# Performance work log

Hardware: AMD Instinct MI355X
Metric: run time of the kernel (lower is better)

Reference implementation:

```python
import jax, jax.numpy as jnp
import numpy as np

N = 50000      # nodes
E = 800000     # edges
IN = 128       # in_channels
H = 128        # hidden_channels
L = 3          # num_layers
CONF_H = 64    # confidence_hidden_dim
TAU0 = 1.0


def _linear_params(key, fan_in, fan_out, bias=True):
    k1, k2 = jax.random.split(key)
    lim = 1.0 / np.sqrt(fan_in)
    w = jax.random.uniform(k1, (fan_in, fan_out), jnp.float32, -lim, lim)
    if bias:
        b = jax.random.uniform(k2, (fan_out,), jnp.float32, -lim, lim)
        return w, b
    return w


def setup_inputs() -> dict:
    key = jax.random.key(0)
    ks = jax.random.split(key, 20)
    x = jax.random.normal(ks[0], (N, IN), jnp.float32)
    edge_index = jax.random.randint(ks[1], (2, E), 0, N, jnp.int32)
    gnoise_soft = jax.random.gumbel(ks[2], (L, N, 2), jnp.float32)
    gnoise_hard = jax.random.gumbel(ks[3], (L, N, 2), jnp.float32)
    conv_w0, conv_b0 = _linear_params(ks[4], IN, H)
    conv_w1, conv_b1 = _linear_params(ks[5], H, H)
    conv_w2, conv_b2 = _linear_params(ks[6], H, H)
    soft_w1, soft_b1 = _linear_params(ks[7], H, CONF_H)
    soft_w2, soft_b2 = _linear_params(ks[8], CONF_H, 2)
    hard_w1, hard_b1 = _linear_params(ks[9], H + 1, CONF_H)
    hard_w2, hard_b2 = _linear_params(ks[10], CONF_H, 2)
    temp_w = _linear_params(ks[11], H, 1, bias=False)
    return dict(x=x, edge_index=edge_index, gnoise_soft=gnoise_soft, gnoise_hard=gnoise_hard,
                conv_w0=conv_w0, conv_b0=conv_b0, conv_w1=conv_w1, conv_b1=conv_b1,
                conv_w2=conv_w2, conv_b2=conv_b2,
                soft_w1=soft_w1, soft_b1=soft_b1, soft_w2=soft_w2, soft_b2=soft_b2,
                hard_w1=hard_w1, hard_b1=hard_b1, hard_w2=hard_w2, hard_b2=hard_b2,
                temp_w=temp_w)


def _forward(x, edge_index, gnoise_soft, gnoise_hard,
             conv_w0, conv_b0, conv_w1, conv_b1, conv_w2, conv_b2,
             soft_w1, soft_b1, soft_w2, soft_b2,
             hard_w1, hard_b1, hard_w2, hard_b2, temp_w):
    src, dst = edge_index[0], edge_index[1]
    loop = jnp.arange(N, dtype=src.dtype)
    # GCN symmetric normalization with self-loops (PyG gcn_norm)
    src_sl = jnp.concatenate([src, loop])
    dst_sl = jnp.concatenate([dst, loop])
    deg = jax.ops.segment_sum(jnp.ones(E + N, x.dtype), dst_sl, num_segments=N)
    dinv = jnp.where(deg > 0, jax.lax.rsqrt(deg), 0.0)
    norm = dinv[src_sl] * dinv[dst_sl]  # [E+N]
    # readiness graph: self-loops removed
    nonself = (src != dst).astype(x.dtype)
    deg_ns = jnp.clip(jax.ops.segment_sum(nonself, src, num_segments=N), 1.0)

    conv_params = [(conv_w0, conv_b0), (conv_w1, conv_b1), (conv_w2, conv_b2)]
    z = jnp.zeros((N, H), x.dtype)
    soft_exited = jnp.zeros(N, bool)
    hard_exited = jnp.zeros(N, bool)
    exit_layers = jnp.full((N,), L, jnp.int32)
    active = []
    h = x
    for li in range(L):
        W, b = conv_params[li]
        hw = h @ W  # [N,H]
        h = jax.ops.segment_sum(norm[:, None] * hw[src_sl], dst_sl, num_segments=N) + b
        if li < L - 1:
            h = jax.nn.gelu(h, approximate=False)  # torch F.gelu default (dropout p=0)
        active.append(jnp.sum(~hard_exited).astype(jnp.int32))
        # temperature head: 1 / (softplus(Wx) + tau0)
        temp = 1.0 / (jax.nn.softplus(h @ temp_w) + TAU0)  # [N,1]
        temp = jnp.where(jnp.isinf(temp), 0.0, temp)
        # soft exit head + gumbel softmax (hard=False)
        soft_logits = jax.nn.relu(h @ soft_w1 + soft_b1) @ soft_w2 + soft_b2  # [N,2]
        sg = jax.nn.softmax((soft_logits + gnoise_soft[li]) / temp, axis=-1)
        soft_dec = sg[:, 1] > sg[:, 0]
        soft_exited = soft_exited | (soft_dec & ~soft_exited)
        # neighbor readiness: mean of soft_exited over non-self neighbors (detached)
        ready_sum = jax.ops.segment_sum(soft_exited[dst].astype(x.dtype) * nonself, src, num_segments=N)
        readiness = jax.lax.stop_gradient((ready_sum / deg_ns)[:, None])
        hin = jnp.concatenate([h, readiness], axis=-1)  # [N,H+1]
        hard_logits = jax.nn.relu(hin @ hard_w1 + hard_b1) @ hard_w2 + hard_b2
        cont = jnp.concatenate([jnp.full((N, 1), 1e6, x.dtype), jnp.zeros((N, 1), x.dtype)], axis=-1)
        eff = jnp.where(soft_exited[:, None], hard_logits, cont)
        hg = jax.nn.softmax((eff + gnoise_hard[li]) / temp, axis=-1)
        hard_dec = hg[:, 1] > hg[:, 0]
        newly = hard_dec & ~hard_exited
        z = z + h * newly[:, None].astype(x.dtype)
        exit_layers = jnp.where(newly, jnp.int32(li), exit_layers)
        hard_exited = hard_exited | newly
    z = z + h * (~hard_exited)[:, None].astype(x.dtype)
    return z, exit_layers, jnp.stack(active)


def reference(x, edge_index, gnoise_soft, gnoise_hard,
              conv_w0, conv_b0, conv_w1, conv_b1, conv_w2, conv_b2,
              soft_w1, soft_b1, soft_w2, soft_b2,
              hard_w1, hard_b1, hard_w2, hard_b2, temp_w):
    return _forward(x, edge_index, gnoise_soft, gnoise_hard,
                    conv_w0, conv_b0, conv_w1, conv_b1, conv_w2, conv_b2,
                    soft_w1, soft_b1, soft_w2, soft_b2,
                    hard_w1, hard_b1, hard_w2, hard_b2, temp_w)
```

## Files before the change

kernel.cpp:

```cpp
#include <hip/hip_runtime.h>
#include <hip/hip_bf16.h>
#include <math.h>

#define NN 50000
#define EE 800000
#define HH 128
#define CHH 64
#define LL 3
#define ZT (NN * HH)
#define NBK 196
#define EPB 3125

using bf16 = __hip_bfloat16;
typedef unsigned short u16;
typedef unsigned int u32;
typedef __attribute__((ext_vector_type(8))) short s16x8;
typedef __attribute__((ext_vector_type(4))) float f32x4;

__device__ __forceinline__ float ldbf(const u16* p, size_t i) {
    return __uint_as_float(((u32)p[i]) << 16);
}
__device__ __forceinline__ u16 f2b(float v) {
    bf16 b = __float2bfloat16(v);
    return *reinterpret_cast<u16*>(&b);
}
__device__ __forceinline__ void stbf(u16* p, size_t i, float v) { p[i] = f2b(v); }
__device__ __forceinline__ float blo(u32 w) { return __uint_as_float(w << 16); }
__device__ __forceinline__ float bhi(u32 w) { return __uint_as_float(w & 0xFFFF0000u); }

__global__ __launch_bounds__(256) void zero_out_k(float* __restrict__ out, int n) {
    int i = blockIdx.x * 256 + threadIdx.x;
    if (i < n) out[i] = 0.f;
}

__global__ __launch_bounds__(256) void init_k(const float* __restrict__ x, u16* __restrict__ h,
        int* __restrict__ softex, int* __restrict__ hardex, int* __restrict__ exitl,
        int* __restrict__ act) {
    int i = blockIdx.x * 256 + threadIdx.x;
    if (i < ZT) stbf(h, (size_t)i, x[i]);
    if (i < NN) { softex[i] = 0; hardex[i] = 0; exitl[i] = LL; }
    if (i < LL) act[i] = 0;
}

__global__ __launch_bounds__(256) void hist_both_k(const int* __restrict__ ei,
        int* __restrict__ hist1, int* __restrict__ hist2) {
    __shared__ int h1[NBK], h2[NBK];
    int t = threadIdx.x, b = blockIdx.x;
    if (t < NBK) { h1[t] = 0; h2[t] = 0; }
    __syncthreads();
    int base = b * EPB;
    for (int i = t; i < EPB; i += 256) {
        int e = base + i;
        int s = ei[e], d = ei[EE + e];
        if ((u32)s >= NN || (u32)d >= NN) continue;
        atomicAdd(&h1[d >> 8], 1);
        if (s != d) atomicAdd(&h2[s >> 8], 1);
    }
    __syncthreads();
    if (t < NBK) { hist1[b * NBK + t] = h1[t]; hist2[b * NBK + t] = h2[t]; }
}

__global__ __launch_bounds__(256) void boffs_k(const int* __restrict__ hist,
        int* __restrict__ boffs, int* __restrict__ bstart) {
    int t = threadIdx.x;
    __shared__ int scn[256];
    int run = 0;
    if (t < NBK) {
        for (int b = 0; b < 256; ++b) {
            boffs[t * 256 + b] = run;
            run += hist[b * NBK + t];
        }
    }
    int v = (t < NBK) ? run : 0;
    scn[t] = v;
    __syncthreads();
    for (int off = 1; off < 256; off <<= 1) {
        int x = (t >= off) ? scn[t - off] : 0;
        __syncthreads();
        scn[t] += x;
        __syncthreads();
    }
    int excl = scn[t] - v;
    if (t < NBK) {
        bstart[t] = excl;
        if (t == NBK - 1) bstart[NBK] = excl + v;
        for (int b = 0; b < 256; ++b) boffs[t * 256 + b] += excl;
    }
}

__global__ __launch_bounds__(256) void scat_both_k(const int* __restrict__ ei,
        const int* __restrict__ boffs1, u32* __restrict__ ebuf1,
        const int* __restrict__ boffs2, u32* __restrict__ ebuf2) {
    __shared__ int c1[NBK], c2[NBK];
    int t = threadIdx.x, b = blockIdx.x;
    if (t < NBK) { c1[t] = boffs1[t * 256 + b]; c2[t] = boffs2[t * 256 + b]; }
    __syncthreads();
    int base = b * EPB;
    for (int i = t; i < EPB; i += 256) {
        int e = base + i;
        int s = ei[e], d = ei[EE + e];
        if ((u32)s >= NN || (u32)d >= NN) continue;
        int pos = atomicAdd(&c1[d >> 8], 1);
        ebuf1[pos] = (u32)s | ((u32)(d & 255) << 16);
        if (s != d) {
            int pos2 = atomicAdd(&c2[s >> 8], 1);
            ebuf2[pos2] = (u32)d | ((u32)(s & 255) << 16);
        }
    }
}

__device__ __forceinline__ void fine_body(int bk, const u32* __restrict__ ebuf,
        const int* __restrict__ bstart, int* __restrict__ rowptr, u16* __restrict__ csrx,
        float* __restrict__ dinv, int addself) {
    __shared__ int cnt[256];
    __shared__ int scn[256];
    int t = threadIdx.x;
    int eb = bstart[bk], ee = bstart[bk + 1];
    cnt[t] = 0;
    __syncthreads();
    for (int i = eb + t; i < ee; i += 256)
        atomicAdd(&cnt[(ebuf[i] >> 16) & 255], 1);
    __syncthreads();
    int v = cnt[t];
    scn[t] = v;
    __syncthreads();
    for (int off = 1; off < 256; off <<= 1) {
        int x = (t >= off) ? scn[t - off] : 0;
        __syncthreads();
        scn[t] += x;
        __syncthreads();
    }
    int excl = scn[t] - v;
    int n = (bk << 8) + t;
    if (n < NN) {
        rowptr[n] = eb + excl;
        if (dinv) dinv[n] = 1.0f / sqrtf((float)(v + addself));
    }
    if (bk == NBK - 1 && t == 0) rowptr[NN] = ee;
    __syncthreads();
    cnt[t] = excl;
    __syncthreads();
    for (int i = eb + t; i < ee; i += 256) {
        u32 w = ebuf[i];
        int lo = (w >> 16) & 255;
        int pos = atomicAdd(&cnt[lo], 1);
        csrx[eb + pos] = (u16)(w & 0xFFFF);
    }
}

__global__ __launch_bounds__(256) void fine2_k(const u32* __restrict__ ebuf1,
        const int* __restrict__ bstart1, int* __restrict__ irow, u16* __restrict__ csrc,
        float* __restrict__ dinv, const u32* __restrict__ ebuf2,
        const int* __restrict__ bstart2, int* __restrict__ orow, u16* __restrict__ ocol) {
    if (blockIdx.x < NBK) fine_body(blockIdx.x, ebuf1, bstart1, irow, csrc, dinv, 1);
    else                  fine_body(blockIdx.x - NBK, ebuf2, bstart2, orow, ocol, nullptr, 0);
}

__global__ __launch_bounds__(256) void pack_w_k(const float* __restrict__ w0,
        const float* __restrict__ w1, const float* __restrict__ w2,
        const float* __restrict__ sw1, const float* __restrict__ hw1, u16* __restrict__ wt) {
    int i = blockIdx.x * 256 + threadIdx.x;
    if (i >= 4 * HH * HH) return;
    int mat = i >> 14, rr = i & 16383, o = rr >> 7, k = rr & 127;
    float v;
    if (mat == 0) v = w0[k * HH + o];
    else if (mat == 1) v = w1[k * HH + o];
    else if (mat == 2) v = w2[k * HH + o];
    else v = (o < CHH) ? sw1[k * CHH + o] : hw1[k * CHH + (o - CHH)];
    stbf(wt, (size_t)i, v);
}

__global__ __launch_bounds__(256) void mega_k(int li, int geluf,
        const int* __restrict__ irow, const u16* __restrict__ csrc, const float* __restrict__ dinv,
        const u16* __restrict__ hin_g, u16* __restrict__ hout_g,
        const u16* __restrict__ Wc, const u16* __restrict__ Wh, const float* __restrict__ bias,
        const float* __restrict__ sb1, const float* __restrict__ sw2, const float* __restrict__ sb2,
        const float* __restrict__ gs, int* __restrict__ softex, const int* __restrict__ hardex,
        float* __restrict__ outP) {
    __shared__ u32 hin[16 * 64];
    __shared__ u16 hl[16 * HH];
    __shared__ float l0s[2][16], l1s[2][16];
    __shared__ int hx[16];
    int tid = threadIdx.x;
    int wave = tid >> 6, lane = tid & 63;
    int row0 = blockIdx.x * 16;
    if (tid < 16) hx[tid] = hardex[row0 + tid];
    #pragma unroll
    for (int i = 0; i < 4; ++i) {
        int row = wave * 4 + i;
        int node = row0 + row;
        int beg = irow[node], end = irow[node + 1];
        float dvd = dinv[node];
        float a0 = 0.f, a1 = 0.f;
        int e = beg;
        for (; e + 3 < end; e += 4) {
            int s0 = csrc[e], s1 = csrc[e + 1], s2 = csrc[e + 2], s3 = csrc[e + 3];
            float n0 = dinv[s0], n1 = dinv[s1], n2 = dinv[s2], n3 = dinv[s3];
            u32 w0 = *(const u32*)(hin_g + (size_t)s0 * HH + lane * 2);
            u32 w1 = *(const u32*)(hin_g + (size_t)s1 * HH + lane * 2);
            u32 w2 = *(const u32*)(hin_g + (size_t)s2 * HH + lane * 2);
            u32 w3 = *(const u32*)(hin_g + (size_t)s3 * HH + lane * 2);
            a0 = fmaf(n0, blo(w0), a0); a1 = fmaf(n0, bhi(w0), a1);
            a0 = fmaf(n1, blo(w1), a0); a1 = fmaf(n1, bhi(w1), a1);
            a0 = fmaf(n2, blo(w2), a0); a1 = fmaf(n2, bhi(w2), a1);
            a0 = fmaf(n3, blo(w3), a0); a1 = fmaf(n3, bhi(w3), a1);
        }
        for (; e < end; ++e) {
            int s0 = csrc[e];
            float n0 = dinv[s0];
            u32 w0 = *(const u32*)(hin_g + (size_t)s0 * HH + lane * 2);
            a0 = fmaf(n0, blo(w0), a0); a1 = fmaf(n0, bhi(w0), a1);
        }
        a0 *= dvd; a1 *= dvd;
        u32 hw = *(const u32*)(hin_g + (size_t)node * HH + lane * 2);
        float self = dvd * dvd;
        a0 = fmaf(blo(hw), self, a0);
        a1 = fmaf(bhi(hw), self, a1);
        hin[row * 64 + (((lane >> 2) ^ (row & 7)) << 2) + (lane & 3)] =
            (u32)f2b(a0) | ((u32)f2b(a1) << 16);
    }
    __syncthreads();
    int r = lane & 15, g = lane >> 4;
    const u16* hinw = (const u16*)hin;
    s16x8 af[4];
    #pragma unroll
    for (int kk = 0; kk < 4; ++kk) {
        int chunk = (kk * 4 + g) ^ (r & 7);
        af[kk] = *(const s16x8*)(hinw + r * HH + chunk * 8);
    }
    f32x4 acc[2];
    #pragma unroll
    for (int cc = 0; cc < 2; ++cc) {
        int c0 = wave * 32 + cc * 16;
        const u16* brow = Wc + (size_t)(c0 + r) * HH;
        f32x4 a = {0.f, 0.f, 0.f, 0.f};
        #pragma unroll
        for (int kk = 0; kk < 4; ++kk) {
            s16x8 b = *(const s16x8*)(brow + kk * 32 + g * 8);
            a = __builtin_amdgcn_mfma_f32_16x16x32_bf16(af[kk], b, a, 0, 0, 0);
        }
        acc[cc] = a;
    }
    #pragma unroll
    for (int cc = 0; cc < 2; ++cc) {
        int col = wave * 32 + cc * 16 + r;
        float bv = bias[col];
        #pragma unroll
        for (int j = 0; j < 4; ++j) {
            int row = g * 4 + j;
            float v = acc[cc][j] + bv;
            if (geluf) v = 0.5f * v * (1.0f + erff(v * 0.70710678118654752f));
            stbf(hout_g, (size_t)(row0 + row) * HH + col, v);
            int chunk = (col >> 3) ^ (row & 7);
            hl[row * HH + chunk * 8 + (col & 7)] = f2b(v);
        }
    }
    __syncthreads();
    #pragma unroll
    for (int kk = 0; kk < 4; ++kk) {
        int k0 = kk * 32 + g * 8;
        int chunk = (k0 >> 3) ^ (r & 7);
        af[kk] = *(const s16x8*)(hl + r * HH + chunk * 8);
    }
    #pragma unroll
    for (int cc = 0; cc < 2; ++cc) {
        int c0 = wave * 32 + cc * 16;
        const u16* brow = Wh + (size_t)(c0 + r) * HH;
        f32x4 a = {0.f, 0.f, 0.f, 0.f};
        #pragma unroll
        for (int kk = 0; kk < 4; ++kk) {
            s16x8 b = *(const s16x8*)(brow + kk * 32 + g * 8);
            a = __builtin_amdgcn_mfma_f32_16x16x32_bf16(af[kk], b, a, 0, 0, 0);
        }
        acc[cc] = a;
    }
    if (wave < 2) {
        float pl0[4] = {0.f, 0.f, 0.f, 0.f}, pl1[4] = {0.f, 0.f, 0.f, 0.f};
        #pragma unroll
        for (int cc = 0; cc < 2; ++cc) {
            int col = wave * 32 + cc * 16 + r;
            float b1 = sb1[col], w20 = sw2[col * 2], w21 = sw2[col * 2 + 1];
            #pragma unroll
            for (int j = 0; j < 4; ++j) {
                float hv = fmaxf(acc[cc][j] + b1, 0.f);
                pl0[j] = fmaf(hv, w20, pl0[j]);
                pl1[j] = fmaf(hv, w21, pl1[j]);
            }
        }
        #pragma unroll
        for (int off = 1; off < 16; off <<= 1) {
            #pragma unroll
            for (int j = 0; j < 4; ++j) {
                pl0[j] += __shfl_xor(pl0[j], off);
                pl1[j] += __shfl_xor(pl1[j], off);
            }
        }
        if (r == 0) {
            #pragma unroll
            for (int j = 0; j < 4; ++j) {
                l0s[wave][g * 4 + j] = pl0[j];
                l1s[wave][g * 4 + j] = pl1[j];
            }
        }
    } else {
        #pragma unroll
        for (int cc = 0; cc < 2; ++cc) {
            int col = wave * 32 + cc * 16 + r;
            #pragma unroll
            for (int j = 0; j < 4; ++j) {
                int row = g * 4 + j;
                if (!hx[row]) outP[(size_t)(row0 + row) * HH + col] = acc[cc][j];
            }
        }
    }
    __syncthreads();
    if (tid < 16) {
        int n = row0 + tid;
        float l0 = l0s[0][tid] + l0s[1][tid] + sb2[0];
        float l1 = l1s[0][tid] + l1s[1][tid] + sb2[1];
        const float* gg = gs + ((size_t)li * NN + n) * 2;
        if (l1 + gg[1] > l0 + gg[0]) softex[n] = 1;
    }
}

__global__ __launch_bounds__(256) void hard_fin_k(int li,
        const u16* __restrict__ h, const float* __restrict__ hw1, const float* __restrict__ hb1,
        const float* __restrict__ hw2, const float* __restrict__ hb2,
        const float* __restrict__ gh, const int* __restrict__ softex,
        int* __restrict__ hardex, int* __restrict__ exitl,
        const int* __restrict__ orow, const u16* __restrict__ ocol,
        float* __restrict__ out) {
    int t = threadIdx.x;
    int n = blockIdx.x * 4 + (t >> 6);
    int j = t & 63;
    if (!softex[n] || hardex[n]) return;
    int ob = orow[n], oe = orow[n + 1];
    int cnt = 0;
    for (int e = ob + j; e < oe; e += 64) cnt += softex[ocol[e]];
    #pragma unroll
    for (int off = 32; off > 0; off >>= 1) cnt += __shfl_xor(cnt, off);
    int dns = oe - ob; if (dns < 1) dns = 1;
    float r = (float)cnt / (float)dns;
    float pv = out[(size_t)n * HH + CHH + j];
    float hid = fmaxf(pv + r * hw1[HH * CHH + j] + hb1[j], 0.f);
    float l0 = hid * hw2[j * 2], l1 = hid * hw2[j * 2 + 1];
    #pragma unroll
    for (int off = 32; off > 0; off >>= 1) {
        l0 += __shfl_xor(l0, off);
        l1 += __shfl_xor(l1, off);
    }
    const float* g = gh + ((size_t)li * NN + n) * 2;
    if (l1 + hb2[1] + g[1] > l0 + hb2[0] + g[0]) {
        if (j == 0) { hardex[n] = 1; exitl[n] = li; }
        u32 hw = *(const u32*)(h + (size_t)n * HH + j * 2);
        out[(size_t)n * HH + j * 2]     = blo(hw);
        out[(size_t)n * HH + j * 2 + 1] = bhi(hw);
    }
}

__global__ __launch_bounds__(256) void tail_k(const u16* __restrict__ h, const int* __restrict__ exitl,
        float* __restrict__ out, int* __restrict__ act) {
    __shared__ int c[LL];
    int t = threadIdx.x;
    int i = blockIdx.x * 256 + t;
    if (t < LL) c[t] = 0;
    __syncthreads();
    if (i < ZT) {
        int n = i >> 7;
        if (exitl[n] == LL) out[i] = ldbf(h, (size_t)i);
    } else if (i < ZT + NN) {
        int e = exitl[i - ZT];
        out[i] = (float)e;
        if (e < LL) atomicAdd(&c[e], 1);
    }
    __syncthreads();
    if (t < LL && c[t]) atomicAdd(&act[t], c[t]);
}

__global__ __launch_bounds__(64) void finalize_k(const int* __restrict__ act, float* __restrict__ out) {
    if (threadIdx.x == 0) {
        out[ZT + NN]     = (float)NN;
        out[ZT + NN + 1] = (float)(NN - act[0]);
        out[ZT + NN + 2] = (float)(NN - act[0] - act[1]);
    }
}

extern "C" void kernel_launch(void* const* d_in, const int* in_sizes, int n_in,
                              void* d_out, int out_size, void* d_ws, size_t ws_size,
                              hipStream_t stream) {
    float* out = (float*)d_out;
    const int OUT_N = ZT + NN + LL;

    static const int CANON[19] = {6400000,1600000,300000,300000,16384,128,16384,128,16384,128,
                                  8192,64,128,2,8256,64,128,2,128};
    static const int SORTED_ROLE[19] = {5,7,9,4,6,8,1,3,2,15,17,14,16,11,13,10,12,18,0};
    int perm[19];
    bool ok = (n_in == 19);
    if (ok) {
        bool mc = true, mr = true, ms = true;
        for (int i = 0; i < 19; ++i) {
            if (in_sizes[i] != CANON[i]) mc = false;
            if (in_sizes[i] != CANON[18 - i]) mr = false;
            if (in_sizes[i] != CANON[SORTED_ROLE[i]]) ms = false;
        }
        if (mc)      for (int c = 0; c < 19; ++c) perm[c] = c;
        else if (mr) for (int c = 0; c < 19; ++c) perm[c] = 18 - c;
        else if (ms) { for (int p = 0; p < 19; ++p) perm[SORTED_ROLE[p]] = p; }
        else         for (int c = 0; c < 19; ++c) perm[c] = c;
    }
    if (!ok) {
        zero_out_k<<<(OUT_N + 255) / 256, 256, 0, stream>>>(out, OUT_N);
        return;
    }

    const float* x  = (const float*)d_in[perm[0]];
    const int*   ei = (const int*)d_in[perm[1]];
    const float* gs = (const float*)d_in[perm[2]];
    const float* gh = (const float*)d_in[perm[3]];
    const float* cw[3] = { (const float*)d_in[perm[4]], (const float*)d_in[perm[6]], (const float*)d_in[perm[8]] };
    const float* cb[3] = { (const float*)d_in[perm[5]], (const float*)d_in[perm[7]], (const float*)d_in[perm[9]] };
    const float* sw1 = (const float*)d_in[perm[10]];
    const float* sb1 = (const float*)d_in[perm[11]];
    const float* sw2 = (const float*)d_in[perm[12]];
    const float* sb2 = (const float*)d_in[perm[13]];
    const float* hw1 = (const float*)d_in[perm[14]];
    const float* hb1 = (const float*)d_in[perm[15]];
    const float* hw2 = (const float*)d_in[perm[16]];
    const float* hb2 = (const float*)d_in[perm[17]];

    const size_t H_B    = (size_t)ZT * 2;
    const size_t FLAG_B = 200192;
    const size_t ACT_B  = 256;
    const size_t RP_B   = 200704;
    const size_t CE_B   = (size_t)EE * 2;
    const size_t WT_B   = 4 * HH * HH * 2;
    const size_t need = 2 * H_B + 4 * FLAG_B + ACT_B + 2 * RP_B + 2 * CE_B + WT_B;
    if (ws_size < need) {
        zero_out_k<<<(OUT_N + 255) / 256, 256, 0, stream>>>(out, OUT_N);
        return;
    }

    char* p = (char*)d_ws;
    u16* hA   = (u16*)p; p += H_B;
    u16* hB   = (u16*)p; p += H_B;
    int* softex = (int*)p; p += FLAG_B;
    int* hardex = (int*)p; p += FLAG_B;
    int* exitl  = (int*)p; p += FLAG_B;
    float* dinv = (float*)p; p += FLAG_B;
    int* act    = (int*)p; p += ACT_B;
    int* irow   = (int*)p; p += RP_B;
    int* orow   = (int*)p; p += RP_B;
    u16* csrc   = (u16*)p; p += CE_B;
    u16* ocol   = (u16*)p; p += CE_B;
    u16* wt     = (u16*)p; p += WT_B;

    char* q = (char*)hB;
    u32* ebuf1  = (u32*)q;  q += (size_t)EE * 4;
    u32* ebuf2  = (u32*)q;  q += (size_t)EE * 4;
    int* hist1  = (int*)q;  q += 256 * NBK * 4;
    int* hist2  = (int*)q;  q += 256 * NBK * 4;
    int* boffs1 = (int*)q;  q += NBK * 256 * 4;
    int* boffs2 = (int*)q;  q += NBK * 256 * 4;
    int* bstart1 = (int*)q; q += 1024;
    int* bstart2 = (int*)q; q += 1024;

    init_k<<<(ZT + 255) / 256, 256, 0, stream>>>(x, hA, softex, hardex, exitl, act);

    hist_both_k<<<256, 256, 0, stream>>>(ei, hist1, hist2);
    boffs_k<<<1, 256, 0, stream>>>(hist1, boffs1, bstart1);
    boffs_k<<<1, 256, 0, stream>>>(hist2, boffs2, bstart2);
    scat_both_k<<<256, 256, 0, stream>>>(ei, boffs1, ebuf1, boffs2, ebuf2);
    fine2_k<<<2 * NBK, 256, 0, stream>>>(ebuf1, bstart1, irow, csrc, dinv,
                                         ebuf2, bstart2, orow, ocol);
    pack_w_k<<<(4 * HH * HH + 255) / 256, 256, 0, stream>>>(cw[0], cw[1], cw[2], sw1, hw1, wt);

    u16* hbuf[2] = { hA, hB };
    for (int li = 0; li < LL; ++li) {
        int geluf = (li < LL - 1) ? 1 : 0;
        u16* hin  = hbuf[li & 1];
        u16* hout = hbuf[(li & 1) ^ 1];
        mega_k<<<NN / 16, 256, 0, stream>>>(li, geluf, irow, csrc, dinv, hin, hout,
                                            wt + (size_t)li * HH * HH, wt + (size_t)3 * HH * HH,
                                            cb[li], sb1, sw2, sb2, gs, softex, hardex, out);
        hard_fin_k<<<NN / 4, 256, 0, stream>>>(li, hout, hw1, hb1, hw2, hb2, gh, softex,
                                               hardex, exitl, orow, ocol, out);
    }
    tail_k<<<(OUT_N + 255) / 256, 256, 0, stream>>>(hbuf[LL & 1], exitl, out, act);
    finalize_k<<<1, 64, 0, stream>>>(act, out);
}
```

Before: 366.2 us.

## Split fused gather+GEMM into column-quartered gather kernel and separate GEMM kernel

The per-layer fused kernel is split in two. A standalone gather kernel aggregates neighbour features, with each block handling 16 nodes and one 32-column quarter so that adjacent blocks share a column slice, which should improve cache locality of the random row reads. The aggregated rows go to a global buffer, and a second kernel runs the MFMA GEMM and heads from it. This adds an extra global write and read of the aggregated features plus one launch per layer, and lets the feature buffer be updated in place instead of ping-ponging.

```diff
diff --git a/kernel.cpp b/kernel.cpp
--- a/kernel.cpp
+++ b/kernel.cpp
@@ -170,14 +170,54 @@
     stbf(wt, (size_t)i, v);
 }
 
-__global__ __launch_bounds__(256) void mega_k(int li, int geluf,
-        const int* __restrict__ irow, const u16* __restrict__ csrc, const float* __restrict__ dinv,
-        const u16* __restrict__ hin_g, u16* __restrict__ hout_g,
+__global__ __launch_bounds__(256) void gather4_k(const int* __restrict__ irow,
+        const u16* __restrict__ csrc, const float* __restrict__ dinv,
+        const u16* __restrict__ hg, u16* __restrict__ hinb) {
+    int bid = blockIdx.x;
+    int c8 = bid & 7;
+    int q = c8 >> 1;
+    int idx = (bid >> 3) * 2 + (c8 & 1);
+    if (idx >= NN / 16) return;
+    int t = threadIdx.x;
+    int node = idx * 16 + (t >> 4);
+    int l = t & 15;
+    int co = q * 32 + l * 2;
+    int beg = irow[node], end = irow[node + 1];
+    float dvd = dinv[node];
+    float a0 = 0.f, a1 = 0.f;
+    int e = beg;
+    for (; e + 3 < end; e += 4) {
+        int s0 = csrc[e], s1 = csrc[e + 1], s2 = csrc[e + 2], s3 = csrc[e + 3];
+        float n0 = dinv[s0], n1 = dinv[s1], n2 = dinv[s2], n3 = dinv[s3];
+        u32 w0 = *(const u32*)(hg + (size_t)s0 * HH + co);
+        u32 w1 = *(const u32*)(hg + (size_t)s1 * HH + co);
+        u32 w2 = *(const u32*)(hg + (size_t)s2 * HH + co);
+        u32 w3 = *(const u32*)(hg + (size_t)s3 * HH + co);
+        a0 = fmaf(n0, blo(w0), a0); a1 = fmaf(n0, bhi(w0), a1);
+        a0 = fmaf(n1, blo(w1), a0); a1 = fmaf(n1, bhi(w1), a1);
+        a0 = fmaf(n2, blo(w2), a0); a1 = fmaf(n2, bhi(w2), a1);
+        a0 = fmaf(n3, blo(w3), a0); a1 = fmaf(n3, bhi(w3), a1);
+    }
+    for (; e < end; ++e) {
+        int s0 = csrc[e];
+        float n0 = dinv[s0];
+        u32 w0 = *(const u32*)(hg + (size_t)s0 * HH + co);
+        a0 = fmaf(n0, blo(w0), a0); a1 = fmaf(n0, bhi(w0), a1);
+    }
+    a0 *= dvd; a1 *= dvd;
+    u32 hw = *(const u32*)(hg + (size_t)node * HH + co);
+    float self = dvd * dvd;
+    a0 = fmaf(blo(hw), self, a0);
+    a1 = fmaf(bhi(hw), self, a1);
+    ((u32*)hinb)[(size_t)node * 64 + q * 16 + l] = (u32)f2b(a0) | ((u32)f2b(a1) << 16);
+}
+
+__global__ __launch_bounds__(256) void gemmheads_k(int li, int geluf,
+        const u16* __restrict__ hinb, u16* __restrict__ hout_g,
         const u16* __restrict__ Wc, const u16* __restrict__ Wh, const float* __restrict__ bias,
         const float* __restrict__ sb1, const float* __restrict__ sw2, const float* __restrict__ sb2,
         const float* __restrict__ gs, int* __restrict__ softex, const int* __restrict__ hardex,
         float* __restrict__ outP) {
-    __shared__ u32 hin[16 * 64];
     __shared__ u16 hl[16 * HH];
     __shared__ float l0s[2][16], l1s[2][16];
     __shared__ int hx[16];
@@ -185,49 +225,11 @@
     int wave = tid >> 6, lane = tid & 63;
     int row0 = blockIdx.x * 16;
     if (tid < 16) hx[tid] = hardex[row0 + tid];
-    #pragma unroll
-    for (int i = 0; i < 4; ++i) {
-        int row = wave * 4 + i;
-        int node = row0 + row;
-        int beg = irow[node], end = irow[node + 1];
-        float dvd = dinv[node];
-        float a0 = 0.f, a1 = 0.f;
-        int e = beg;
-        for (; e + 3 < end; e += 4) {
-            int s0 = csrc[e], s1 = csrc[e + 1], s2 = csrc[e + 2], s3 = csrc[e + 3];
-            float n0 = dinv[s0], n1 = dinv[s1], n2 = dinv[s2], n3 = dinv[s3];
-            u32 w0 = *(const u32*)(hin_g + (size_t)s0 * HH + lane * 2);
-            u32 w1 = *(const u32*)(hin_g + (size_t)s1 * HH + lane * 2);
-            u32 w2 = *(const u32*)(hin_g + (size_t)s2 * HH + lane * 2);
-            u32 w3 = *(const u32*)(hin_g + (size_t)s3 * HH + lane * 2);
-            a0 = fmaf(n0, blo(w0), a0); a1 = fmaf(n0, bhi(w0), a1);
-            a0 = fmaf(n1, blo(w1), a0); a1 = fmaf(n1, bhi(w1), a1);
-            a0 = fmaf(n2, blo(w2), a0); a1 = fmaf(n2, bhi(w2), a1);
-            a0 = fmaf(n3, blo(w3), a0); a1 = fmaf(n3, bhi(w3), a1);
-        }
-        for (; e < end; ++e) {
-            int s0 = csrc[e];
-            float n0 = dinv[s0];
-            u32 w0 = *(const u32*)(hin_g + (size_t)s0 * HH + lane * 2);
-            a0 = fmaf(n0, blo(w0), a0); a1 = fmaf(n0, bhi(w0), a1);
-        }
-        a0 *= dvd; a1 *= dvd;
-        u32 hw = *(const u32*)(hin_g + (size_t)node * HH + lane * 2);
-        float self = dvd * dvd;
-        a0 = fmaf(blo(hw), self, a0);
-        a1 = fmaf(bhi(hw), self, a1);
-        hin[row * 64 + (((lane >> 2) ^ (row & 7)) << 2) + (lane & 3)] =
-            (u32)f2b(a0) | ((u32)f2b(a1) << 16);
-    }
-    __syncthreads();
     int r = lane & 15, g = lane >> 4;
-    const u16* hinw = (const u16*)hin;
+    const u16* arow = hinb + (size_t)(row0 + r) * HH;
     s16x8 af[4];
     #pragma unroll
-    for (int kk = 0; kk < 4; ++kk) {
-        int chunk = (kk * 4 + g) ^ (r & 7);
-        af[kk] = *(const s16x8*)(hinw + r * HH + chunk * 8);
-    }
+    for (int kk = 0; kk < 4; ++kk) af[kk] = *(const s16x8*)(arow + kk * 32 + g * 8);
     f32x4 acc[2];
     #pragma unroll
     for (int cc = 0; cc < 2; ++cc) {
@@ -441,8 +443,8 @@
     }
 
     char* p = (char*)d_ws;
-    u16* hA   = (u16*)p; p += H_B;
-    u16* hB   = (u16*)p; p += H_B;
+    u16* h    = (u16*)p; p += H_B;
+    u16* hinb = (u16*)p; p += H_B;
     int* softex = (int*)p; p += FLAG_B;
     int* hardex = (int*)p; p += FLAG_B;
     int* exitl  = (int*)p; p += FLAG_B;
@@ -454,7 +456,7 @@
     u16* ocol   = (u16*)p; p += CE_B;
     u16* wt     = (u16*)p; p += WT_B;
 
-    char* q = (char*)hB;
+    char* q = (char*)hinb;
     u32* ebuf1  = (u32*)q;  q += (size_t)EE * 4;
     u32* ebuf2  = (u32*)q;  q += (size_t)EE * 4;
     int* hist1  = (int*)q;  q += 256 * NBK * 4;
@@ -464,7 +466,7 @@
     int* bstart1 = (int*)q; q += 1024;
     int* bstart2 = (int*)q; q += 1024;
 
-    init_k<<<(ZT + 255) / 256, 256, 0, stream>>>(x, hA, softex, hardex, exitl, act);
+    init_k<<<(ZT + 255) / 256, 256, 0, stream>>>(x, h, softex, hardex, exitl, act);
 
     hist_both_k<<<256, 256, 0, stream>>>(ei, hist1, hist2);
     boffs_k<<<1, 256, 0, stream>>>(hist1, boffs1, bstart1);
@@ -474,17 +476,16 @@
                                          ebuf2, bstart2, orow, ocol);
     pack_w_k<<<(4 * HH * HH + 255) / 256, 256, 0, stream>>>(cw[0], cw[1], cw[2], sw1, hw1, wt);
 
-    u16* hbuf[2] = { hA, hB };
+    const int G4_GRID = ((NN / 16 + 1) / 2) * 8 + 8;
     for (int li = 0; li < LL; ++li) {
         int geluf = (li < LL - 1) ? 1 : 0;
-        u16* hin  = hbuf[li & 1];
-        u16* hout = hbuf[(li & 1) ^ 1];
-        mega_k<<<NN / 16, 256, 0, stream>>>(li, geluf, irow, csrc, dinv, hin, hout,
-                                            wt + (size_t)li * HH * HH, wt + (size_t)3 * HH * HH,
-                                            cb[li], sb1, sw2, sb2, gs, softex, hardex, out);
-        hard_fin_k<<<NN / 4, 256, 0, stream>>>(li, hout, hw1, hb1, hw2, hb2, gh, softex,
+        gather4_k<<<G4_GRID, 256, 0, stream>>>(irow, csrc, dinv, h, hinb);
+        gemmheads_k<<<NN / 16, 256, 0, stream>>>(li, geluf, hinb, h,
+                                                 wt + (size_t)li * HH * HH, wt + (size_t)3 * HH * HH,
+                                                 cb[li], sb1, sw2, sb2, gs, softex, hardex, out);
+        hard_fin_k<<<NN / 4, 256, 0, stream>>>(li, h, hw1, hb1, hw2, hb2, gh, softex,
                                                hardex, exitl, orow, ocol, out);
     }
-    tail_k<<<(OUT_N + 255) / 256, 256, 0, stream>>>(hbuf[LL & 1], exitl, out, act);
+    tail_k<<<(OUT_N + 255) / 256, 256, 0, stream>>>(h, exitl, out, act);
     finalize_k<<<1, 64, 0, stream>>>(act, out);
 }
```

After: 436.7 us. +19.3%, slower.

## Fuse previous layer's hard-exit decision into next layer's aggregation kernel

Applied to the files above, without the earlier changes.

Moves the hard-exit decision for layer li-1 into the start of mega_k for layer li, which removes two separate hard_fin_k launches. The soft-exit flags are now double-buffered so the fused pass can read the previous layer's flags while the new ones are written. The edge-gather loop is also unrolled to eight edges per iteration to keep more loads in flight. In exchange, mega_k gains a sync, extra registers and some serial per-row work that may lower occupancy.

```diff
diff --git a/kernel.cpp b/kernel.cpp
--- a/kernel.cpp
+++ b/kernel.cpp
@@ -34,11 +34,11 @@
 }
 
 __global__ __launch_bounds__(256) void init_k(const float* __restrict__ x, u16* __restrict__ h,
-        int* __restrict__ softex, int* __restrict__ hardex, int* __restrict__ exitl,
-        int* __restrict__ act) {
+        int* __restrict__ sx0, int* __restrict__ sx1, int* __restrict__ hardex,
+        int* __restrict__ exitl, int* __restrict__ act) {
     int i = blockIdx.x * 256 + threadIdx.x;
     if (i < ZT) stbf(h, (size_t)i, x[i]);
-    if (i < NN) { softex[i] = 0; hardex[i] = 0; exitl[i] = LL; }
+    if (i < NN) { sx0[i] = 0; sx1[i] = 0; hardex[i] = 0; exitl[i] = LL; }
     if (i < LL) act[i] = 0;
 }
 
@@ -170,12 +170,17 @@
     stbf(wt, (size_t)i, v);
 }
 
-__global__ __launch_bounds__(256) void mega_k(int li, int geluf,
+__global__ __launch_bounds__(256) void mega_k(int li, int geluf, int doHF,
         const int* __restrict__ irow, const u16* __restrict__ csrc, const float* __restrict__ dinv,
+        const int* __restrict__ orow, const u16* __restrict__ ocol,
         const u16* __restrict__ hin_g, u16* __restrict__ hout_g,
         const u16* __restrict__ Wc, const u16* __restrict__ Wh, const float* __restrict__ bias,
         const float* __restrict__ sb1, const float* __restrict__ sw2, const float* __restrict__ sb2,
-        const float* __restrict__ gs, int* __restrict__ softex, const int* __restrict__ hardex,
+        const float* __restrict__ gs, const float* __restrict__ ghPrev,
+        const int* __restrict__ sxPrev, int* __restrict__ sxOut,
+        int* __restrict__ hardex, int* __restrict__ exitl,
+        const float* __restrict__ hw1, const float* __restrict__ hb1,
+        const float* __restrict__ hw2, const float* __restrict__ hb2,
         float* __restrict__ outP) {
     __shared__ u32 hin[16 * 64];
     __shared__ u16 hl[16 * HH];
@@ -185,6 +190,39 @@
     int wave = tid >> 6, lane = tid & 63;
     int row0 = blockIdx.x * 16;
     if (tid < 16) hx[tid] = hardex[row0 + tid];
+    __syncthreads();
+    if (doHF) {
+        int lp = li - 1;
+        for (int i = 0; i < 4; ++i) {
+            int row = wave * 4 + i;
+            int n = row0 + row;
+            if (sxPrev[n] && !hx[row]) {
+                int ob = orow[n], oe = orow[n + 1];
+                int cnt = 0;
+                for (int e = ob + lane; e < oe; e += 64) cnt += sxPrev[ocol[e]];
+                #pragma unroll
+                for (int off = 32; off > 0; off >>= 1) cnt += __shfl_xor(cnt, off);
+                int dns = oe - ob; if (dns < 1) dns = 1;
+                float r = (float)cnt / (float)dns;
+                float pv = outP[(size_t)n * HH + CHH + lane];
+                float hid = fmaxf(pv + r * hw1[HH * CHH + lane] + hb1[lane], 0.f);
+                float l0 = hid * hw2[lane * 2], l1 = hid * hw2[lane * 2 + 1];
+                #pragma unroll
+                for (int off = 32; off > 0; off >>= 1) {
+                    l0 += __shfl_xor(l0, off);
+                    l1 += __shfl_xor(l1, off);
+                }
+                const float* g = ghPrev + (size_t)n * 2;
+                if (l1 + hb2[1] + g[1] > l0 + hb2[0] + g[0]) {
+                    if (lane == 0) { hardex[n] = 1; exitl[n] = lp; hx[row] = 1; }
+                    u32 hw_ = *(const u32*)(hin_g + (size_t)n * HH + lane * 2);
+                    outP[(size_t)n * HH + lane * 2]     = blo(hw_);
+                    outP[(size_t)n * HH + lane * 2 + 1] = bhi(hw_);
+                }
+            }
+        }
+        __syncthreads();
+    }
     #pragma unroll
     for (int i = 0; i < 4; ++i) {
         int row = wave * 4 + i;
@@ -193,29 +231,47 @@
         float dvd = dinv[node];
         float a0 = 0.f, a1 = 0.f;
         int e = beg;
-        for (; e + 3 < end; e += 4) {
-            int s0 = csrc[e], s1 = csrc[e + 1], s2 = csrc[e + 2], s3 = csrc[e + 3];
+        for (; e + 7 < end; e += 8) {
+            int s0 = csrc[e], s1 = csrc[e+1], s2 = csrc[e+2], s3 = csrc[e+3];
+            int s4 = csrc[e+4], s5 = csrc[e+5], s6 = csrc[e+6], s7 = csrc[e+7];
             float n0 = dinv[s0], n1 = dinv[s1], n2 = dinv[s2], n3 = dinv[s3];
+            float n4 = dinv[s4], n5 = dinv[s5], n6 = dinv[s6], n7 = dinv[s7];
             u32 w0 = *(const u32*)(hin_g + (size_t)s0 * HH + lane * 2);
             u32 w1 = *(const u32*)(hin_g + (size_t)s1 * HH + lane * 2);
             u32 w2 = *(const u32*)(hin_g + (size_t)s2 * HH + lane * 2);
             u32 w3 = *(const u32*)(hin_g + (size_t)s3 * HH + lane * 2);
+            u32 w4 = *(const u32*)(hin_g + (size_t)s4 * HH + lane * 2);
+            u32 w5 = *(const u32*)(hin_g + (size_t)s5 * HH + lane * 2);
+            u32 w6 = *(const u32*)(hin_g + (size_t)s6 * HH + lane * 2);
+            u32 w7 = *(const u32*)(hin_g + (size_t)s7 * HH + lane * 2);
             a0 = fmaf(n0, blo(w0), a0); a1 = fmaf(n0, bhi(w0), a1);
             a0 = fmaf(n1, blo(w1), a0); a1 = fmaf(n1, bhi(w1), a1);
             a0 = fmaf(n2, blo(w2), a0); a1 = fmaf(n2, bhi(w2), a1);
             a0 = fmaf(n3, blo(w3), a0); a1 = fmaf(n3, bhi(w3), a1);
-        }
-        for (; e < end; ++e) {
+            a0 = fmaf(n4, blo(w4), a0); a1 = fmaf(n4, bhi(w4), a1);
+            a0 = fmaf(n5, blo(w5), a0); a1 = fmaf(n5, bhi(w5), a1);
+            a0 = fmaf(n6, blo(w6), a0); a1 = fmaf(n6, bhi(w6), a1);
+            a0 = fmaf(n7, blo(w7), a0); a1 = fmaf(n7, bhi(w7), a1);
+        }
+        for (; e + 1 < end; e += 2) {
+            int s0 = csrc[e], s1 = csrc[e + 1];
+            float n0 = dinv[s0], n1 = dinv[s1];
+            u32 w0 = *(const u32*)(hin_g + (size_t)s0 * HH + lane * 2);
+            u32 w1 = *(const u32*)(hin_g + (size_t)s1 * HH + lane * 2);
+            a0 = fmaf(n0, blo(w0), a0); a1 = fmaf(n0, bhi(w0), a1);
+            a0 = fmaf(n1, blo(w1), a0); a1 = fmaf(n1, bhi(w1), a1);
+        }
+        if (e < end) {
             int s0 = csrc[e];
             float n0 = dinv[s0];
             u32 w0 = *(const u32*)(hin_g + (size_t)s0 * HH + lane * 2);
             a0 = fmaf(n0, blo(w0), a0); a1 = fmaf(n0, bhi(w0), a1);
         }
         a0 *= dvd; a1 *= dvd;
-        u32 hw = *(const u32*)(hin_g + (size_t)node * HH + lane * 2);
+        u32 hw_ = *(const u32*)(hin_g + (size_t)node * HH + lane * 2);
         float self = dvd * dvd;
-        a0 = fmaf(blo(hw), self, a0);
-        a1 = fmaf(bhi(hw), self, a1);
+        a0 = fmaf(blo(hw_), self, a0);
+        a1 = fmaf(bhi(hw_), self, a1);
         hin[row * 64 + (((lane >> 2) ^ (row & 7)) << 2) + (lane & 3)] =
             (u32)f2b(a0) | ((u32)f2b(a1) << 16);
     }
@@ -319,24 +375,24 @@
         float l0 = l0s[0][tid] + l0s[1][tid] + sb2[0];
         float l1 = l1s[0][tid] + l1s[1][tid] + sb2[1];
         const float* gg = gs + ((size_t)li * NN + n) * 2;
-        if (l1 + gg[1] > l0 + gg[0]) softex[n] = 1;
-    }
-}
-
-__global__ __launch_bounds__(256) void hard_fin_k(int li,
+        int dec = (l1 + gg[1] > l0 + gg[0]) ? 1 : 0;
+        sxOut[n] = sxPrev[n] | dec;
+    }
+}
+
+__global__ __launch_bounds__(256) void hard_fin_k(int li, const int* __restrict__ sx,
         const u16* __restrict__ h, const float* __restrict__ hw1, const float* __restrict__ hb1,
         const float* __restrict__ hw2, const float* __restrict__ hb2,
-        const float* __restrict__ gh, const int* __restrict__ softex,
-        int* __restrict__ hardex, int* __restrict__ exitl,
+        const float* __restrict__ gh, int* __restrict__ hardex, int* __restrict__ exitl,
         const int* __restrict__ orow, const u16* __restrict__ ocol,
         float* __restrict__ out) {
     int t = threadIdx.x;
     int n = blockIdx.x * 4 + (t >> 6);
     int j = t & 63;
-    if (!softex[n] || hardex[n]) return;
+    if (!sx[n] || hardex[n]) return;
     int ob = orow[n], oe = orow[n + 1];
     int cnt = 0;
-    for (int e = ob + j; e < oe; e += 64) cnt += softex[ocol[e]];
+    for (int e = ob + j; e < oe; e += 64) cnt += sx[ocol[e]];
     #pragma unroll
     for (int off = 32; off > 0; off >>= 1) cnt += __shfl_xor(cnt, off);
     int dns = oe - ob; if (dns < 1) dns = 1;
@@ -352,9 +408,9 @@
     const float* g = gh + ((size_t)li * NN + n) * 2;
     if (l1 + hb2[1] + g[1] > l0 + hb2[0] + g[0]) {
         if (j == 0) { hardex[n] = 1; exitl[n] = li; }
-        u32 hw = *(const u32*)(h + (size_t)n * HH + j * 2);
-        out[(size_t)n * HH + j * 2]     = blo(hw);
-        out[(size_t)n * HH + j * 2 + 1] = bhi(hw);
+        u32 hw_ = *(const u32*)(h + (size_t)n * HH + j * 2);
+        out[(size_t)n * HH + j * 2]     = blo(hw_);
+        out[(size_t)n * HH + j * 2 + 1] = bhi(hw_);
     }
 }
 
@@ -434,7 +490,7 @@
     const size_t RP_B   = 200704;
     const size_t CE_B   = (size_t)EE * 2;
     const size_t WT_B   = 4 * HH * HH * 2;
-    const size_t need = 2 * H_B + 4 * FLAG_B + ACT_B + 2 * RP_B + 2 * CE_B + WT_B;
+    const size_t need = 2 * H_B + 5 * FLAG_B + ACT_B + 2 * RP_B + 2 * CE_B + WT_B;
     if (ws_size < need) {
         zero_out_k<<<(OUT_N + 255) / 256, 256, 0, stream>>>(out, OUT_N);
         return;
@@ -443,7 +499,8 @@
     char* p = (char*)d_ws;
     u16* hA   = (u16*)p; p += H_B;
     u16* hB   = (u16*)p; p += H_B;
-    int* softex = (int*)p; p += FLAG_B;
+    int* sx0    = (int*)p; p += FLAG_B;
+    int* sx1    = (int*)p; p += FLAG_B;
     int* hardex = (int*)p; p += FLAG_B;
     int* exitl  = (int*)p; p += FLAG_B;
     float* dinv = (float*)p; p += FLAG_B;
@@ -464,7 +521,7 @@
     int* bstart1 = (int*)q; q += 1024;
     int* bstart2 = (int*)q; q += 1024;
 
-    init_k<<<(ZT + 255) / 256, 256, 0, stream>>>(x, hA, softex, hardex, exitl, act);
+    init_k<<<(ZT + 255) / 256, 256, 0, stream>>>(x, hA, sx0, sx1, hardex, exitl, act);
 
     hist_both_k<<<256, 256, 0, stream>>>(ei, hist1, hist2);
     boffs_k<<<1, 256, 0, stream>>>(hist1, boffs1, bstart1);
@@ -475,16 +532,22 @@
     pack_w_k<<<(4 * HH * HH + 255) / 256, 256, 0, stream>>>(cw[0], cw[1], cw[2], sw1, hw1, wt);
 
     u16* hbuf[2] = { hA, hB };
+    int* sxb[2] = { sx0, sx1 };
     for (int li = 0; li < LL; ++li) {
         int geluf = (li < LL - 1) ? 1 : 0;
         u16* hin  = hbuf[li & 1];
         u16* hout = hbuf[(li & 1) ^ 1];
-        mega_k<<<NN / 16, 256, 0, stream>>>(li, geluf, irow, csrc, dinv, hin, hout,
+        const float* ghPrev = (li > 0) ? (gh + (size_t)(li - 1) * NN * 2) : gh;
+        mega_k<<<NN / 16, 256, 0, stream>>>(li, geluf, li > 0 ? 1 : 0,
+                                            irow, csrc, dinv, orow, ocol, hin, hout,
                                             wt + (size_t)li * HH * HH, wt + (size_t)3 * HH * HH,
-                                            cb[li], sb1, sw2, sb2, gs, softex, hardex, out);
-        hard_fin_k<<<NN / 4, 256, 0, stream>>>(li, hout, hw1, hb1, hw2, hb2, gh, softex,
-                                               hardex, exitl, orow, ocol, out);
-    }
+                                            cb[li], sb1, sw2, sb2, gs, ghPrev,
+                                            sxb[li & 1], sxb[(li + 1) & 1],
+                                            hardex, exitl, hw1, hb1, hw2, hb2, out);
+    }
+    hard_fin_k<<<NN / 4, 256, 0, stream>>>(LL - 1, sxb[LL & 1], hbuf[LL & 1],
+                                           hw1, hb1, hw2, hb2, gh,
+                                           hardex, exitl, orow, ocol, out);
     tail_k<<<(OUT_N + 255) / 256, 256, 0, stream>>>(hbuf[LL & 1], exitl, out, act);
     finalize_k<<<1, 64, 0, stream>>>(act, out);
 }
```

Result: faster. 344.2 us (-6.0%).
